# Performance work log

Measured on AMD Instinct MI355X. Metric: run time of the kernel, lower is better.

Reference implementation:

```python
import jax, jax.numpy as jnp
import numpy as np

CHEB_K = 3

def avwgcn(x, E, W_pool, b_pool):
    # x: [B,N,Cin], E: [N,e], W_pool: [e,K,Cin,Cout], b_pool: [e,Cout]
    N = E.shape[0]
    A = jax.nn.softmax(jax.nn.relu(E @ E.T), axis=1)          # adaptive adjacency [N,N]
    supports = [jnp.eye(N, dtype=x.dtype), A]
    for _ in range(2, CHEB_K):
        supports.append(2.0 * (A @ supports[-1]) - supports[-2])
    S = jnp.stack(supports)                                    # [K,N,N]
    W = jnp.einsum('ne,ekio->nkio', E, W_pool)                 # per-node weights
    b = E @ b_pool                                             # [N,Cout]
    xg = jnp.einsum('knm,bmi->bnki', S, x)                     # Chebyshev graph conv
    return jnp.einsum('bnki,nkio->bno', xg, W) + b


def setup_inputs() -> dict:
    key = jax.random.key(0)
    ks = jax.random.split(key, 7)
    B, N, Din, Dout, E_DIM = 64, 1024, 64, 64, 16
    C = Din + Dout
    return {
        'x': jax.random.normal(ks[0], (B, N, Din), dtype=jnp.float32),
        'state': jax.random.normal(ks[1], (B, N, Dout), dtype=jnp.float32),
        'node_embeddings': jax.random.normal(ks[2], (N, E_DIM), dtype=jnp.float32),
        'gate_W_pool': jax.random.normal(ks[3], (E_DIM, CHEB_K, C, 2 * Dout), dtype=jnp.float32) * 0.1,
        'gate_b_pool': jax.random.normal(ks[4], (E_DIM, 2 * Dout), dtype=jnp.float32) * 0.1,
        'upd_W_pool': jax.random.normal(ks[5], (E_DIM, CHEB_K, C, Dout), dtype=jnp.float32) * 0.1,
        'upd_b_pool': jax.random.normal(ks[6], (E_DIM, Dout), dtype=jnp.float32) * 0.1,
    }


def reference(x, state, node_embeddings, gate_W_pool, gate_b_pool, upd_W_pool, upd_b_pool):
    hidden_dim = state.shape[-1]
    input_and_state = jnp.concatenate([x, state], axis=-1)
    z_r = jax.nn.sigmoid(avwgcn(input_and_state, node_embeddings, gate_W_pool, gate_b_pool))
    z, r = z_r[..., :hidden_dim], z_r[..., hidden_dim:]
    candidate = jnp.concatenate([x, z * state], axis=-1)
    hc = jnp.tanh(avwgcn(candidate, node_embeddings, upd_W_pool, upd_b_pool))
    return r * state + (1.0 - r) * hc
```

## Files before the change

kernel.cpp:

```cpp
#include <hip/hip_runtime.h>
#include <math.h>

#define N_NODES 1024
#define B_SZ 64
#define GNH 4096
#define KI 384
#define EDIM 16
#define WG_NODE 49152
#define WG_WAVE 12288
#define WU_NODE 24576
#define WU_WAVE 6144

typedef _Float16 half8_t __attribute__((ext_vector_type(8)));
typedef float f32x4 __attribute__((ext_vector_type(4)));

__device__ __forceinline__ unsigned short f2h(float f) {
    _Float16 h = (_Float16)f;
    return *(unsigned short*)&h;
}
__device__ __forceinline__ float h2f(unsigned short u) {
    _Float16 h = *(_Float16*)&u;
    return (float)h;
}
__device__ __forceinline__ float sigmoidf_(float v) {
    return 1.f / (1.f + __expf(-v));
}
__device__ __forceinline__ void load_lds16(const void* g, void* l) {
    __builtin_amdgcn_global_load_lds(
        (const __attribute__((address_space(1))) void*)g,
        (__attribute__((address_space(3))) void*)l, 16, 0, 0);
}

__global__ __launch_bounds__(256) void compute_A_kernel(
    const float* __restrict__ E, unsigned short* __restrict__ Ah) {
    __shared__ float red[256];
    const int tid = threadIdx.x;
    const int n = blockIdx.x;
    float en[EDIM];
#pragma unroll
    for (int e = 0; e < EDIM; ++e) en[e] = E[n * EDIM + e];
    float logit[4], lmax = -1e30f;
#pragma unroll
    for (int j = 0; j < 4; ++j) {
        const int m = tid + j * 256;
        float d = 0.f;
#pragma unroll
        for (int e = 0; e < EDIM; ++e) d += en[e] * E[m * EDIM + e];
        d = fmaxf(d, 0.f);
        logit[j] = d;
        lmax = fmaxf(lmax, d);
    }
    red[tid] = lmax;
    __syncthreads();
    for (int s = 128; s > 0; s >>= 1) {
        if (tid < s) red[tid] = fmaxf(red[tid], red[tid + s]);
        __syncthreads();
    }
    lmax = red[0];
    __syncthreads();
    float ex[4], lsum = 0.f;
#pragma unroll
    for (int j = 0; j < 4; ++j) {
        ex[j] = __expf(logit[j] - lmax);
        lsum += ex[j];
    }
    red[tid] = lsum;
    __syncthreads();
    for (int s = 128; s > 0; s >>= 1) {
        if (tid < s) red[tid] += red[tid + s];
        __syncthreads();
    }
    const float inv = 1.f / red[0];
#pragma unroll
    for (int j = 0; j < 4; ++j)
        Ah[n * N_NODES + tid + j * 256] = f2h(ex[j] * inv);
}

__global__ __launch_bounds__(256) void build_T0_all_kernel(
    const float* __restrict__ x, const float* __restrict__ state,
    unsigned short* __restrict__ TX0, unsigned short* __restrict__ TS0,
    unsigned short* __restrict__ TX0T, unsigned short* __restrict__ TS0T) {
    __shared__ unsigned short Lx[64 * 72];
    __shared__ unsigned short Lss[64 * 72];
    const int tid = threadIdx.x;
    const int n0 = blockIdx.x * 64;
    const int b = blockIdx.y;
#pragma unroll
    for (int t = 0; t < 16; ++t) {
        const int id = t * 256 + tid;
        const int nl = id >> 6;
        const int c = id & 63;
        const float xv = x[((size_t)b * N_NODES + n0 + nl) * 64 + c];
        const float sv = state[((size_t)b * N_NODES + n0 + nl) * 64 + c];
        const unsigned short xh = f2h(xv), sh = f2h(sv);
        TX0[(size_t)(n0 + nl) * GNH + b * 64 + c] = xh;
        TS0[(size_t)(n0 + nl) * GNH + b * 64 + c] = sh;
        Lx[c * 72 + nl] = xh;
        Lss[c * 72 + nl] = sh;
    }
    __syncthreads();
#pragma unroll
    for (int t = 0; t < 2; ++t) {
        const int id = t * 256 + tid;
        const int c = id >> 3;
        const int n8 = id & 7;
        uint4 xv = *(const uint4*)&Lx[c * 72 + n8 * 8];
        uint4 sv = *(const uint4*)&Lss[c * 72 + n8 * 8];
        *(uint4*)&TX0T[(size_t)(b * 64 + c) * N_NODES + n0 + n8 * 8] = xv;
        *(uint4*)&TS0T[(size_t)(b * 64 + c) * N_NODES + n0 + n8 * 8] = sv;
    }
}

__global__ __launch_bounds__(256) void transpose16_kernel(
    const unsigned short* __restrict__ src, unsigned short* __restrict__ dst,
    int W) {
    __shared__ unsigned short Ls[64 * 72];
    const int tid = threadIdx.x;
    const int r0 = blockIdx.x * 64;
    const int c0 = blockIdx.y * 64;
#pragma unroll
    for (int t = 0; t < 2; ++t) {
        const int id = t * 256 + tid;
        const int row = id >> 3;
        const int c8 = id & 7;
        uint4 v = *(const uint4*)&src[(size_t)(r0 + row) * W + c0 + c8 * 8];
        const unsigned short* vp = (const unsigned short*)&v;
#pragma unroll
        for (int j = 0; j < 8; ++j) Ls[(c8 * 8 + j) * 72 + row] = vp[j];
    }
    __syncthreads();
#pragma unroll
    for (int t = 0; t < 2; ++t) {
        const int id = t * 256 + tid;
        const int c = id >> 3;
        const int r8 = id & 7;
        uint4 v = *(const uint4*)&Ls[c * 72 + r8 * 8];
        *(uint4*)&dst[(size_t)(c0 + c) * N_NODES + r0 + r8 * 8] = v;
    }
}

__global__ __launch_bounds__(256) void gemm_s2_kernel(
    const unsigned short* __restrict__ Ah,
    const unsigned short* __restrict__ AhT, unsigned short* __restrict__ S2h) {
    __shared__ unsigned short As[64 * 64];
    __shared__ unsigned short Bs[64 * 64];
    const int tid = threadIdx.x;
    const int wave = tid >> 6;
    const int lane = tid & 63;
    const int l15 = lane & 15;
    const int quad = lane >> 4;
    const int n0 = blockIdx.x * 64;
    const int m0 = blockIdx.y * 64;
    const int wn = wave * 16;
    const int lr = lane >> 3;
    const int lsw = (lane & 7) ^ lr;

    f32x4 acc[4] = {};
    for (int k0 = 0; k0 < N_NODES; k0 += 64) {
#pragma unroll
        for (int i = 0; i < 2; ++i) {
            const int rbase = (wave * 2 + i) * 8;
            load_lds16(&Ah[(size_t)(n0 + rbase + lr) * N_NODES + k0 + lsw * 8],
                       &As[rbase * 64]);
            load_lds16(&AhT[(size_t)(m0 + rbase + lr) * N_NODES + k0 + lsw * 8],
                       &Bs[rbase * 64]);
        }
        __syncthreads();
#pragma unroll
        for (int ks = 0; ks < 2; ++ks) {
            const int slot = ((ks * 4 + quad) ^ (l15 & 7)) * 8;
            const half8_t b = *(const half8_t*)&Bs[(wn + l15) * 64 + slot];
#pragma unroll
            for (int mi = 0; mi < 4; ++mi) {
                const half8_t a = *(const half8_t*)&As[(mi * 16 + l15) * 64 + slot];
                acc[mi] =
                    __builtin_amdgcn_mfma_f32_16x16x32_f16(a, b, acc[mi], 0, 0, 0);
            }
        }
        __syncthreads();
    }
#pragma unroll
    for (int mi = 0; mi < 4; ++mi) {
#pragma unroll
        for (int r = 0; r < 4; ++r) {
            const int n_g = n0 + mi * 16 + quad * 4 + r;
            const int m_g = m0 + wn + l15;
            const float v = 2.f * acc[mi][r] - (n_g == m_g ? 1.f : 0.f);
            S2h[(size_t)n_g * N_NODES + m_g] = f2h(v);
        }
    }
}

template <int BM>
__global__ __launch_bounds__(512, 2) void gemm_graph8_kernel(
    const unsigned short* __restrict__ Ah,
    const unsigned short* __restrict__ S2h,
    const unsigned short* __restrict__ BTX,
    const unsigned short* __restrict__ BTS,
    unsigned short* __restrict__ T1X, unsigned short* __restrict__ T1S,
    unsigned short* __restrict__ T2X, unsigned short* __restrict__ T2S,
    int ysplit, int colsPerXcd) {
    constexpr int MFR = BM / 32;
    constexpr int ASLOT_H = BM * 32;
    constexpr int SLOT_H = ASLOT_H + 8192;
    constexpr int APASS = BM / 128;
    constexpr int MT = 2048 / BM;
    __shared__ unsigned short lds[4 * SLOT_H];

    const int tid = threadIdx.x;
    const int wave = tid >> 6;
    const int lane = tid & 63;
    const int l15 = lane & 15;
    const int quad = lane >> 4;
    const int wm = (wave >> 2) * (BM / 2);
    const int wn = (wave & 3) * 64;

    const int id = blockIdx.x;
    const int xcd = id & 7;
    const int j = id >> 3;
    const int mtile = j & (MT - 1);
    const int ytile = xcd * colsPerXcd + j / MT;
    const int mrow0 = mtile * BM;
    const bool isA = mrow0 < N_NODES;
    const unsigned short* Asrc =
        (isA ? Ah : S2h) + (size_t)(mrow0 & 1023) * N_NODES;
    const bool isX = ytile < ysplit;
    const int col0 = (isX ? ytile : ytile - ysplit) * 256;
    const unsigned short* Bsrc = (isX ? BTX : BTS) + (size_t)col0 * N_NODES;
    unsigned short* OUT = (isA ? (isX ? T1X : T1S) : (isX ? T2X : T2S)) +
                          (size_t)(mrow0 & 1023) * GNH + col0;

    int goff[2];
#pragma unroll
    for (int jp = 0; jp < 2; ++jp) {
        const int cell = jp * 512 + tid;
        const int prow = cell >> 3;
        const int q = (cell & 7) ^ (prow & 7);
        goff[jp] = (2 * prow + (q >> 2)) * N_NODES + (q & 3) * 8;
    }

    int offA[MFR], offB[4];
#pragma unroll
    for (int mi = 0; mi < MFR; ++mi) {
        const int prow = (wm >> 1) + mi * 8 + (l15 >> 1);
        const int s8 = ((l15 & 1) * 4 + quad) ^ (prow & 7);
        offA[mi] = prow * 64 + s8 * 8;
    }
#pragma unroll
    for (int ni = 0; ni < 4; ++ni) {
        const int pcol = (wn >> 1) + ni * 8 + (l15 >> 1);
        const int s8 = ((l15 & 1) * 4 + quad) ^ (pcol & 7);
        offB[ni] = ASLOT_H + pcol * 64 + s8 * 8;
    }

    f32x4 acc[MFR][4] = {};

    auto stageA = [&](int t) {
        const int sl = t & 3;
#pragma unroll
        for (int jp = 0; jp < APASS; ++jp)
            load_lds16(Asrc + (size_t)t * 32 + goff[jp],
                       &lds[sl * SLOT_H + jp * 4096 + wave * 512]);
    };
    auto stageB = [&](int t) {
        const int sl = t & 3;
#pragma unroll
        for (int jp = 0; jp < 2; ++jp)
            load_lds16(Bsrc + (size_t)t * 32 + goff[jp],
                       &lds[sl * SLOT_H + ASLOT_H + jp * 4096 + wave * 512]);
    };
    auto waitPipe = [&] {
        if constexpr (BM == 256)
            asm volatile("s_waitcnt vmcnt(8)" ::: "memory");
        else
            asm volatile("s_waitcnt vmcnt(6)" ::: "memory");
    };

    auto tileBody = [&](int t, bool tail) {
        const unsigned short* base = &lds[(t & 3) * SLOT_H];
        half8_t a[MFR], b0, b1, b2, b3;
#pragma unroll
        for (int mi = 0; mi < MFR; ++mi)
            a[mi] = *(const half8_t*)&base[offA[mi]];
        b0 = *(const half8_t*)&base[offB[0]];
        b1 = *(const half8_t*)&base[offB[1]];
        if (!tail) stageA(t + 3);
        __builtin_amdgcn_sched_barrier(0);
        __builtin_amdgcn_s_barrier();
        asm volatile("s_waitcnt lgkmcnt(0)" ::: "memory");
        __builtin_amdgcn_sched_barrier(0);
        __builtin_amdgcn_s_setprio(1);
#pragma unroll
        for (int mi = 0; mi < MFR; ++mi) {
            acc[mi][0] = __builtin_amdgcn_mfma_f32_16x16x32_f16(
                a[mi], b0, acc[mi][0], 0, 0, 0);
            acc[mi][1] = __builtin_amdgcn_mfma_f32_16x16x32_f16(
                a[mi], b1, acc[mi][1], 0, 0, 0);
        }
        __builtin_amdgcn_s_setprio(0);
        __builtin_amdgcn_sched_barrier(0);
        __builtin_amdgcn_s_barrier();
        b2 = *(const half8_t*)&base[offB[2]];
        b3 = *(const half8_t*)&base[offB[3]];
        if (!tail) {
            stageB(t + 3);
            waitPipe();
        } else {
            asm volatile("s_waitcnt vmcnt(0)" ::: "memory");
        }
        __builtin_amdgcn_sched_barrier(0);
        __builtin_amdgcn_s_barrier();
        asm volatile("s_waitcnt lgkmcnt(0)" ::: "memory");
        __builtin_amdgcn_sched_barrier(0);
        __builtin_amdgcn_s_setprio(1);
#pragma unroll
        for (int mi = 0; mi < MFR; ++mi) {
            acc[mi][2] = __builtin_amdgcn_mfma_f32_16x16x32_f16(
                a[mi], b2, acc[mi][2], 0, 0, 0);
            acc[mi][3] = __builtin_amdgcn_mfma_f32_16x16x32_f16(
                a[mi], b3, acc[mi][3], 0, 0, 0);
        }
        __builtin_amdgcn_s_setprio(0);
        __builtin_amdgcn_sched_barrier(0);
        __builtin_amdgcn_s_barrier();
    };

    stageA(0); stageB(0);
    stageA(1); stageB(1);
    stageA(2); stageB(2);
    waitPipe();
    __builtin_amdgcn_s_barrier();
    __builtin_amdgcn_sched_barrier(0);

#pragma unroll 4
    for (int t = 0; t < 28; ++t) tileBody(t, false);
    tileBody(28, false);
    tileBody(29, true);
    tileBody(30, true);
    tileBody(31, true);

    constexpr int NPASS = BM / 64;
#pragma unroll
    for (int p = 0; p < NPASS; ++p) {
        __syncthreads();
        const int whalf = (BM == 256) ? (p >> 1) : p;
        const int mi0 = (BM == 256) ? (p & 1) * 4 : 0;
        if ((wave >> 2) == whalf) {
#pragma unroll
            for (int mi = 0; mi < 4; ++mi)
#pragma unroll
                for (int ni = 0; ni < 4; ++ni)
#pragma unroll
                    for (int r = 0; r < 4; ++r) {
                        const int row = mi * 16 + quad * 4 + r;
                        const int col = wn + ni * 16 + l15;
                        lds[row * 264 + col] = f2h(acc[mi0 + mi][ni][r]);
                    }
        }
        __syncthreads();
#pragma unroll
        for (int i = 0; i < 4; ++i) {
            const int id2 = i * 512 + tid;
            const int row = id2 >> 5;
            const int c8 = id2 & 31;
            uint4 v = *(const uint4*)&lds[row * 264 + c8 * 8];
            *(uint4*)&OUT[(size_t)(p * 64 + row) * GNH + c8 * 8] = v;
        }
    }
}

__global__ __launch_bounds__(256) void dequant_gate_kernel(
    const float* __restrict__ Wp, const float* __restrict__ E,
    unsigned short* __restrict__ Wt) {
    __shared__ float En[32 * 16];
    const int tid = threadIdx.x;
    const int c8 = blockIdx.x * 256 + tid;
    const int n0 = blockIdx.y * 32;
    const int sub = c8 & 1;
    const int c = c8 >> 1;
    const int l15 = c & 15;
    const int quad = (c >> 4) & 3;
    const int half = (c >> 6) & 1;
    const int ks = (c >> 7) & 3;
    const int sq = c >> 9;
    const int s = sq % 3;
    const int w = sq / 3;
    const int k0 = s * 128 + (ks * 4 + quad) * 8 + sub * 4;
    const int o = w * 32 + half * 16 + l15;

#pragma unroll
    for (int t = 0; t < 2; ++t) {
        const int id = t * 256 + tid;
        En[id] = E[(n0 + (id >> 4)) * EDIM + (id & 15)];
    }
    __syncthreads();

    f32x4 wv[EDIM];
#pragma unroll
    for (int e = 0; e < EDIM; ++e) {
        f32x4 v;
#pragma unroll
        for (int j = 0; j < 4; ++j)
            v[j] = Wp[(size_t)(e * KI + k0 + j) * 128 + o];
        wv[e] = v;
    }

#pragma unroll 4
    for (int nl = 0; nl < 32; ++nl) {
        f32x4 a = {0.f, 0.f, 0.f, 0.f};
#pragma unroll
        for (int e = 0; e < EDIM; ++e) a += wv[e] * En[nl * EDIM + e];
        union { unsigned short u[4]; uint2 v; } pk;
#pragma unroll
        for (int j = 0; j < 4; ++j) pk.u[j] = f2h(a[j]);
        *(uint2*)&Wt[(size_t)(n0 + nl) * WG_NODE + (size_t)c8 * 4] = pk.v;
    }
}

__global__ __launch_bounds__(256) void dequant_upd_kernel(
    const float* __restrict__ Wp, const float* __restrict__ E,
    unsigned short* __restrict__ Wt) {
    __shared__ float En[32 * 16];
    const int tid = threadIdx.x;
    const int c8 = blockIdx.x * 256 + tid;
    const int n0 = blockIdx.y * 32;
    const int sub = c8 & 1;
    const int c = c8 >> 1;
    const int l15 = c & 15;
    const int quad = (c >> 4) & 3;
    const int ks = (c >> 6) & 3;
    const int sq = c >> 8;
    const int s = sq % 3;
    const int w = sq / 3;
    const int k0 = s * 128 + (ks * 4 + quad) * 8 + sub * 4;
    const int o = w * 16 + l15;

#pragma unroll
    for (int t = 0; t < 2; ++t) {
        const int id = t * 256 + tid;
        En[id] = E[(n0 + (id >> 4)) * EDIM + (id & 15)];
    }
    __syncthreads();

    f32x4 wv[EDIM];
#pragma unroll
    for (int e = 0; e < EDIM; ++e) {
        f32x4 v;
#pragma unroll
        for (int j = 0; j < 4; ++j)
            v[j] = Wp[(size_t)(e * KI + k0 + j) * 64 + o];
        wv[e] = v;
    }

#pragma unroll 4
    for (int nl = 0; nl < 32; ++nl) {
        f32x4 a = {0.f, 0.f, 0.f, 0.f};
#pragma unroll
        for (int e = 0; e < EDIM; ++e) a += wv[e] * En[nl * EDIM + e];
        union { unsigned short u[4]; uint2 v; } pk;
#pragma unroll
        for (int j = 0; j < 4; ++j) pk.u[j] = f2h(a[j]);
        *(uint2*)&Wt[(size_t)(n0 + nl) * WU_NODE + (size_t)c8 * 4] = pk.v;
    }
}

__global__ __launch_bounds__(256) void pernode_gate_kernel(
    const unsigned short* __restrict__ TX0,
    const unsigned short* __restrict__ TS0,
    const unsigned short* __restrict__ TX1,
    const unsigned short* __restrict__ TS1,
    const unsigned short* __restrict__ TX2,
    const unsigned short* __restrict__ TS2,
    const unsigned short* __restrict__ Wt, const float* __restrict__ E,
    const float* __restrict__ bp, const float* __restrict__ state,
    unsigned short* __restrict__ rbuf, unsigned short* __restrict__ cand) {
    __shared__ unsigned short XsX[64 * 64];
    __shared__ unsigned short XsS[64 * 64];
    const int n = blockIdx.x;
    const int tid = threadIdx.x;
    const int wave = tid >> 6;
    const int lane = tid & 63;
    const int l15 = lane & 15;
    const int quad = lane >> 4;
    const int wn = wave * 32;
    const int lr = lane >> 3;
    const int lsw = (lane & 7) ^ lr;

    float bias[2];
#pragma unroll
    for (int ni = 0; ni < 2; ++ni) {
        float bv = 0.f;
#pragma unroll
        for (int e = 0; e < EDIM; ++e)
            bv += E[n * EDIM + e] * bp[e * 128 + wn + ni * 16 + l15];
        bias[ni] = bv;
    }

    f32x4 acc[4][2] = {};

    const unsigned short* TXs[3] = {TX0, TX1, TX2};
    const unsigned short* TSs[3] = {TS0, TS1, TS2};
    const unsigned short* wbase =
        Wt + ((size_t)n * 4 + wave) * WG_WAVE + lane * 8;

    for (int s = 0; s < 3; ++s) {
        const unsigned short* xs = TXs[s] + (size_t)n * GNH;
        const unsigned short* ss = TSs[s] + (size_t)n * GNH;
#pragma unroll
        for (int i = 0; i < 2; ++i) {
            const int slab = wave * 2 + i;
            load_lds16(xs + (slab * 8 + lr) * 64 + lsw * 8, &XsX[slab * 512]);
            load_lds16(ss + (slab * 8 + lr) * 64 + lsw * 8, &XsS[slab * 512]);
        }
        __syncthreads();
#pragma unroll
        for (int ks = 0; ks < 4; ++ks) {
            const int kseg = ks * 4 + quad;
            half8_t b[2];
            b[0] = *(const half8_t*)&wbase[((s * 4 + ks) * 2 + 0) * 512];
            b[1] = *(const half8_t*)&wbase[((s * 4 + ks) * 2 + 1) * 512];
            const unsigned short* plane = (kseg < 8) ? XsX : XsS;
            const int aslot = ((kseg & 7) ^ (l15 & 7)) * 8;
#pragma unroll
            for (int mi = 0; mi < 4; ++mi) {
                const half8_t a =
                    *(const half8_t*)&plane[(mi * 16 + l15) * 64 + aslot];
#pragma unroll
                for (int ni = 0; ni < 2; ++ni)
                    acc[mi][ni] = __builtin_amdgcn_mfma_f32_16x16x32_f16(
                        a, b[ni], acc[mi][ni], 0, 0, 0);
            }
        }
        __syncthreads();
    }

#pragma unroll
    for (int mi = 0; mi < 4; ++mi) {
#pragma unroll
        for (int r = 0; r < 4; ++r) {
            const int b_g = mi * 16 + quad * 4 + r;
#pragma unroll
            for (int ni = 0; ni < 2; ++ni) {
                const int o_g = wn + ni * 16 + l15;
                const float v = sigmoidf_(acc[mi][ni][r] + bias[ni]);
                if (o_g < 64) {
                    const float sv =
                        state[((size_t)b_g * N_NODES + n) * 64 + o_g];
                    cand[(size_t)n * GNH + b_g * 64 + o_g] = f2h(v * sv);
                } else {
                    rbuf[((size_t)n * B_SZ + b_g) * 64 + (o_g - 64)] = f2h(v);
                }
            }
        }
    }
}

__global__ __launch_bounds__(256) void pernode_upd_kernel(
    const unsigned short* __restrict__ TX0,
    const unsigned short* __restrict__ CAND,
    const unsigned short* __restrict__ TX1,
    const unsigned short* __restrict__ TS1,
    const unsigned short* __restrict__ TX2,
    const unsigned short* __restrict__ TS2,
    const unsigned short* __restrict__ Wt, const float* __restrict__ E,
    const float* __restrict__ bp, const float* __restrict__ state,
    const unsigned short* __restrict__ rbuf, float* __restrict__ out) {
    __shared__ unsigned short XsX[64 * 64];
    __shared__ unsigned short XsS[64 * 64];
    const int n = blockIdx.x;
    const int tid = threadIdx.x;
    const int wave = tid >> 6;
    const int lane = tid & 63;
    const int l15 = lane & 15;
    const int quad = lane >> 4;
    const int wn = wave * 16;
    const int o_g = wn + l15;
    const int lr = lane >> 3;
    const int lsw = (lane & 7) ^ lr;

    float bias = 0.f;
#pragma unroll
    for (int e = 0; e < EDIM; ++e)
        bias += E[n * EDIM + e] * bp[e * 64 + o_g];

    f32x4 acc[4] = {};

    const unsigned short* TXs[3] = {TX0, TX1, TX2};
    const unsigned short* TSs[3] = {CAND, TS1, TS2};
    const unsigned short* wbase =
        Wt + ((size_t)n * 4 + wave) * WU_WAVE + lane * 8;

    for (int s = 0; s < 3; ++s) {
        const unsigned short* xs = TXs[s] + (size_t)n * GNH;
        const unsigned short* ss = TSs[s] + (size_t)n * GNH;
#pragma unroll
        for (int i = 0; i < 2; ++i) {
            const int slab = wave * 2 + i;
            load_lds16(xs + (slab * 8 + lr) * 64 + lsw * 8, &XsX[slab * 512]);
            load_lds16(ss + (slab * 8 + lr) * 64 + lsw * 8, &XsS[slab * 512]);
        }
        __syncthreads();
#pragma unroll
        for (int ks = 0; ks < 4; ++ks) {
            const int kseg = ks * 4 + quad;
            const half8_t b = *(const half8_t*)&wbase[(s * 4 + ks) * 512];
            const unsigned short* plane = (kseg < 8) ? XsX : XsS;
            const int aslot = ((kseg & 7) ^ (l15 & 7)) * 8;
#pragma unroll
            for (int mi = 0; mi < 4; ++mi) {
                const half8_t a =
                    *(const half8_t*)&plane[(mi * 16 + l15) * 64 + aslot];
                acc[mi] = __builtin_amdgcn_mfma_f32_16x16x32_f16(a, b, acc[mi],
                                                                 0, 0, 0);
            }
        }
        __syncthreads();
    }

#pragma unroll
    for (int mi = 0; mi < 4; ++mi) {
#pragma unroll
        for (int r = 0; r < 4; ++r) {
            const int b_g = mi * 16 + quad * 4 + r;
            const float hc = tanhf(acc[mi][r] + bias);
            const float rr = h2f(rbuf[((size_t)n * B_SZ + b_g) * 64 + o_g]);
            const float sv = state[((size_t)b_g * N_NODES + n) * 64 + o_g];
            out[((size_t)b_g * N_NODES + n) * 64 + o_g] =
                rr * sv + (1.f - rr) * hc;
        }
    }
}

extern "C" void kernel_launch(void* const* d_in, const int* in_sizes, int n_in,
                              void* d_out, int out_size, void* d_ws,
                              size_t ws_size, hipStream_t stream) {
    const float* x = (const float*)d_in[0];
    const float* state = (const float*)d_in[1];
    const float* E = (const float*)d_in[2];
    const float* gW = (const float*)d_in[3];
    const float* gb = (const float*)d_in[4];
    const float* uW = (const float*)d_in[5];
    const float* ub = (const float*)d_in[6];
    float* out = (float*)d_out;

    char* ws = (char*)d_ws;
    unsigned short* Ah = (unsigned short*)ws;
    unsigned short* AhT = (unsigned short*)(ws + 2097152);
    unsigned short* S2h = (unsigned short*)(ws + 4194304);
    unsigned short* TX0 = (unsigned short*)(ws + 6291456);
    unsigned short* TS0 = (unsigned short*)(ws + 14680064);
    unsigned short* TX0T = (unsigned short*)(ws + 23068672);
    unsigned short* TS0T = (unsigned short*)(ws + 31457280);
    unsigned short* TX1 = (unsigned short*)(ws + 39845888);
    unsigned short* TS1 = (unsigned short*)(ws + 48234496);
    unsigned short* TX2 = (unsigned short*)(ws + 56623104);
    unsigned short* TS2 = (unsigned short*)(ws + 65011712);
    unsigned short* Wt = (unsigned short*)(ws + 73400320);
    unsigned short* rbuf = (unsigned short*)(ws + 174063616);
    unsigned short* CAND = (unsigned short*)(ws + 182452224);

    compute_A_kernel<<<N_NODES, 256, 0, stream>>>(E, Ah);
    build_T0_all_kernel<<<dim3(16, 64), 256, 0, stream>>>(x, state, TX0, TS0,
                                                          TX0T, TS0T);
    transpose16_kernel<<<dim3(16, 16), 256, 0, stream>>>(Ah, AhT, N_NODES);
    gemm_s2_kernel<<<dim3(16, 16), 256, 0, stream>>>(Ah, AhT, S2h);

    gemm_graph8_kernel<256><<<256, 512, 0, stream>>>(
        Ah, S2h, TX0T, TS0T, TX1, TS1, TX2, TS2, 16, 4);
    dequant_gate_kernel<<<dim3(48, 32), 256, 0, stream>>>(gW, E, Wt);
    pernode_gate_kernel<<<N_NODES, 256, 0, stream>>>(
        TX0, TS0, TX1, TS1, TX2, TS2, Wt, E, gb, state, rbuf, CAND);
    transpose16_kernel<<<dim3(16, 64), 256, 0, stream>>>(CAND, TS0T, GNH);

    gemm_graph8_kernel<128><<<256, 512, 0, stream>>>(
        Ah, S2h, TX0T, TS0T, TX1, TS1, TX2, TS2, 0, 2);
    dequant_upd_kernel<<<dim3(24, 32), 256, 0, stream>>>(uW, E, Wt);
    pernode_upd_kernel<<<N_NODES, 256, 0, stream>>>(
        TX0, CAND, TX1, TS1, TX2, TS2, Wt, E, ub, state, rbuf, out);
}
```

Baseline: 277.2 us.

## Merge split MFMA half-phases into one phase per K-tile, dropping extra barriers

The GEMM main loop used to split each K-tile into two halves (B fragments 0-1, then 2-3), each wrapped in its own workgroup barriers, with A and B staging interleaved between them. It now loads all four B fragments up front, issues both the A and B global-to-LDS stages for tile t+3 together, runs all MFMAs in a single prioritized block, and keeps only the one barrier at the end of the tile. The goal is to cut three of the four s_barrier synchronizations per tile and the waits that come with them. In exchange, more fragment registers are live at once, and waves lose the barrier-enforced interleaving of memory issue and MFMA work, which may reduce overlap. Reuse of the 4-slot LDS ring still depends on the single end-of-tile barrier.

```diff
diff --git a/kernel.cpp b/kernel.cpp
--- a/kernel.cpp
+++ b/kernel.cpp
@@ -278,49 +278,34 @@
 
     auto tileBody = [&](int t, bool tail) {
         const unsigned short* base = &lds[(t & 3) * SLOT_H];
-        half8_t a[MFR], b0, b1, b2, b3;
+        half8_t a[MFR], b[4];
 #pragma unroll
         for (int mi = 0; mi < MFR; ++mi)
             a[mi] = *(const half8_t*)&base[offA[mi]];
-        b0 = *(const half8_t*)&base[offB[0]];
-        b1 = *(const half8_t*)&base[offB[1]];
-        if (!tail) stageA(t + 3);
+#pragma unroll
+        for (int ni = 0; ni < 4; ++ni)
+            b[ni] = *(const half8_t*)&base[offB[ni]];
+        if (!tail) {
+            stageA(t + 3);
+            stageB(t + 3);
+        }
         __builtin_amdgcn_sched_barrier(0);
-        __builtin_amdgcn_s_barrier();
         asm volatile("s_waitcnt lgkmcnt(0)" ::: "memory");
         __builtin_amdgcn_sched_barrier(0);
         __builtin_amdgcn_s_setprio(1);
 #pragma unroll
-        for (int mi = 0; mi < MFR; ++mi) {
-            acc[mi][0] = __builtin_amdgcn_mfma_f32_16x16x32_f16(
-                a[mi], b0, acc[mi][0], 0, 0, 0);
-            acc[mi][1] = __builtin_amdgcn_mfma_f32_16x16x32_f16(
-                a[mi], b1, acc[mi][1], 0, 0, 0);
-        }
+        for (int mi = 0; mi < MFR; ++mi)
+#pragma unroll
+            for (int ni = 0; ni < 4; ++ni)
+                acc[mi][ni] = __builtin_amdgcn_mfma_f32_16x16x32_f16(
+                    a[mi], b[ni], acc[mi][ni], 0, 0, 0);
         __builtin_amdgcn_s_setprio(0);
         __builtin_amdgcn_sched_barrier(0);
-        __builtin_amdgcn_s_barrier();
-        b2 = *(const half8_t*)&base[offB[2]];
-        b3 = *(const half8_t*)&base[offB[3]];
         if (!tail) {
-            stageB(t + 3);
             waitPipe();
         } else {
             asm volatile("s_waitcnt vmcnt(0)" ::: "memory");
         }
-        __builtin_amdgcn_sched_barrier(0);
-        __builtin_amdgcn_s_barrier();
-        asm volatile("s_waitcnt lgkmcnt(0)" ::: "memory");
-        __builtin_amdgcn_sched_barrier(0);
-        __builtin_amdgcn_s_setprio(1);
-#pragma unroll
-        for (int mi = 0; mi < MFR; ++mi) {
-            acc[mi][2] = __builtin_amdgcn_mfma_f32_16x16x32_f16(
-                a[mi], b2, acc[mi][2], 0, 0, 0);
-            acc[mi][3] = __builtin_amdgcn_mfma_f32_16x16x32_f16(
-                a[mi], b3, acc[mi][3], 0, 0, 0);
-        }
-        __builtin_amdgcn_s_setprio(0);
         __builtin_amdgcn_sched_barrier(0);
         __builtin_amdgcn_s_barrier();
     };
```

Result: no change. 276.1 us (-0.4%).
